# Performance work log

Hardware: AMD Instinct MI355X
Metric: run time of the kernel (lower is better)

## Reference

```python
import jax, jax.numpy as jnp
import numpy as np

N_NODES = 16384
FM = 256
N_EDGES = 524288


def gcn_conv(x, W, b, edge_index, edge_weight):
    """PyG GCNConv: y = D^-1/2 (A+I) D^-1/2 (x @ W) + b, with edge weights."""
    n = x.shape[0]
    loop = jnp.arange(n)
    src = jnp.concatenate([edge_index[0], loop])
    dst = jnp.concatenate([edge_index[1], loop])
    w = jnp.concatenate([edge_weight, jnp.ones((n,), edge_weight.dtype)])
    deg = jax.ops.segment_sum(w, dst, num_segments=n)
    dinv = jnp.where(deg > 0, jax.lax.rsqrt(jnp.maximum(deg, 1e-30)), 0.0)
    norm = dinv[src] * w * dinv[dst]            # [E+n]
    h = x @ W                                    # [n, fm]
    msg = h[src] * norm[:, None]                 # [E+n, fm] gather
    return jax.ops.segment_sum(msg, dst, num_segments=n) + b


def setup_inputs() -> dict:
    key = jax.random.key(0)
    ks = jax.random.split(key, 24)
    inp = {
        "x": jax.random.normal(ks[0], (N_NODES, FM), jnp.float32),
        "edges_f": jax.random.randint(ks[1], (2, N_EDGES), 0, N_NODES),
        "ew_f": jax.random.uniform(ks[2], (N_EDGES,), jnp.float32),
        "edges_s": jax.random.randint(ks[3], (2, N_EDGES), 0, N_NODES),
        "ew_s": jax.random.uniform(ks[4], (N_EDGES,), jnp.float32),
        "edges_g": jax.random.randint(ks[5], (2, N_EDGES), 0, N_NODES),
        "ew_g": jax.random.uniform(ks[6], (N_EDGES,), jnp.float32),
    }
    names = ["f1", "f2", "s1", "s2", "g1", "g2"]
    for i, nm in enumerate(names):
        inp["W" + nm] = 0.05 * jax.random.normal(ks[7 + i], (FM, FM), jnp.float32)
        inp["b" + nm] = jnp.zeros((FM,), jnp.float32)
    inp["fc1_w"] = 0.5 * jax.random.normal(ks[13], (30, 6), jnp.float32)
    inp["fc1_b"] = jnp.zeros((30,), jnp.float32)
    inp["fc2_w"] = 0.5 * jax.random.normal(ks[14], (6, 30), jnp.float32)
    inp["fc2_b"] = jnp.zeros((6,), jnp.float32)
    inp["cnn_w"] = 0.5 * jax.random.normal(ks[15], (6,), jnp.float32)
    inp["cnn_b"] = jnp.zeros((1,), jnp.float32)
    return inp


def reference(x, edges_f, ew_f, edges_s, ew_s, edges_g, ew_g,
              Wf1, bf1, Wf2, bf2, Ws1, bs1, Ws2, bs2, Wg1, bg1, Wg2, bg2,
              fc1_w, fc1_b, fc2_w, fc2_b, cnn_w, cnn_b):
    # three 2-layer GCN branches with relu
    f1 = jax.nn.relu(gcn_conv(x, Wf1, bf1, edges_f, ew_f))
    f2 = jax.nn.relu(gcn_conv(f1, Wf2, bf2, edges_f, ew_f))
    s1 = jax.nn.relu(gcn_conv(x, Ws1, bs1, edges_s, ew_s))
    s2 = jax.nn.relu(gcn_conv(s1, Ws2, bs2, edges_s, ew_s))
    g1 = jax.nn.relu(gcn_conv(x, Wg1, bg1, edges_g, ew_g))
    g2 = jax.nn.relu(gcn_conv(g1, Wg2, bg2, edges_g, ew_g))
    # cat along features then t().view(1,6,fm,N) == stack of transposed branches
    XM = jnp.stack([f1.T, f2.T, s1.T, s2.T, g1.T, g2.T])  # [6, fm, N]
    # SE channel attention
    pooled = jnp.mean(XM, axis=(1, 2))                     # [6]
    h = jax.nn.relu(fc1_w @ pooled + fc1_b)                # [30]
    att = jax.nn.sigmoid(fc2_w @ h + fc2_b)                # [6]
    XM_att = jax.nn.relu(att[:, None, None] * XM)          # [6, fm, N]
    # 1x1 conv 6->1 channels
    out = jnp.einsum('c,cfn->fn', cnn_w, XM_att) + cnn_b[0]  # [fm, N]
    return out.T                                            # [N, fm]
```

## Files before the change

kernel.cpp:

```cpp
#include <hip/hip_runtime.h>
#include <hip/hip_bf16.h>

#define N_NODES 16384
#define FM      256
#define NF      (N_NODES * FM)
#define NF4     (NF / 4)
#define NPART   8
#define NSCAN   (NPART * N_NODES)
#define RS_STRIDE 131076
#define NRS_STRIDE (N_NODES + 2)
#define NCHUNK 128
#define NCHUNK_N 16

typedef __attribute__((ext_vector_type(8))) short short8;
typedef __attribute__((ext_vector_type(8))) ushort ushort8;
typedef __attribute__((ext_vector_type(4))) float f32x4;

__device__ inline ushort f2bf(float f) {
    uint u = __float_as_uint(f);
    return (ushort)((u + 0x7FFFu + ((u >> 16) & 1u)) >> 16);
}
__device__ inline uint pack2bf(float a, float b) {
    return (uint)f2bf(a) | ((uint)f2bf(b) << 16);
}
__device__ inline float bf2f(ushort u) { return __uint_as_float(((uint)u) << 16); }

__global__ void init_kernel(int* __restrict__ cnt3, float* __restrict__ pooled) {
    int i = blockIdx.x * blockDim.x + threadIdx.x;
    int n = 3 * NSCAN;
    if (i < n) cnt3[i] = 0;
    else if (i < n + 6) pooled[i - n] = 0.0f;
}

__global__ void cnt_edges_all(const int* __restrict__ d0, const int* __restrict__ d1,
                              const int* __restrict__ d2,
                              int* __restrict__ cnt3, int E) {
    int t = blockIdx.y;
    const int* dst = (t == 0) ? d0 : (t == 1) ? d1 : d2;
    int part = blockIdx.x & (NPART - 1);
    int* cnt = cnt3 + t * NSCAN + part * N_NODES;
    int e = blockIdx.x * blockDim.x + threadIdx.x;
    if (e < E) atomicAdd(&cnt[dst[e]], 1);
}


__global__ void tot_kernel(const int* __restrict__ cnt3, int* __restrict__ tot3) {
    int i = blockIdx.x * blockDim.x + threadIdx.x;
    if (i >= 3 * N_NODES) return;
    int set = i / N_NODES;
    int node = i - set * N_NODES;
    const int* cnt = cnt3 + set * NSCAN;
    int s = 0;
#pragma unroll
    for (int p = 0; p < NPART; ++p) s += cnt[p * N_NODES + node];
    tot3[i] = s;
}

__global__ __launch_bounds__(1024) void chunk_sum(const int* __restrict__ src,
                                                  long set_stride,
                                                  int* __restrict__ psum,
                                                  int nchunk) {
    int set = blockIdx.y;
    const int* p = src + (size_t)set * set_stride + (size_t)blockIdx.x * 1024;
    __shared__ int lds[1024];
    int t = threadIdx.x;
    lds[t] = p[t];
    __syncthreads();
    for (int off = 512; off > 0; off >>= 1) {
        if (t < off) lds[t] += lds[t + off];
        __syncthreads();
    }
    if (t == 0) psum[set * nchunk + blockIdx.x] = lds[0];
}

__global__ __launch_bounds__(128) void scan_chunks(int* __restrict__ psum,
                                                   int* __restrict__ npsum) {
    __shared__ int lds[128];
    int t = threadIdx.x;
    for (int set = 0; set < 3; ++set) {
        int v = psum[set * NCHUNK + t];
        lds[t] = v;
        __syncthreads();
        for (int off = 1; off < 128; off <<= 1) {
            int u = (t >= off) ? lds[t - off] : 0;
            __syncthreads();
            lds[t] += u;
            __syncthreads();
        }
        psum[set * NCHUNK + t] = lds[t] - v;
        __syncthreads();
    }
    for (int set = 0; set < 3; ++set) {
        int v = (t < NCHUNK_N) ? npsum[set * NCHUNK_N + t] : 0;
        lds[t] = v;
        __syncthreads();
        for (int off = 1; off < NCHUNK_N; off <<= 1) {
            int u = (t >= off && t < NCHUNK_N) ? lds[t - off] : 0;
            __syncthreads();
            if (t < NCHUNK_N) lds[t] += u;
            __syncthreads();
        }
        if (t < NCHUNK_N) npsum[set * NCHUNK_N + t] = lds[t] - v;
        __syncthreads();
    }
}

__global__ __launch_bounds__(1024) void scan_write_rs(const int* __restrict__ cnt3,
                                                      const int* __restrict__ psum,
                                                      int* __restrict__ rowstart3,
                                                      int* __restrict__ cursor3) {
    int set = blockIdx.y;
    int base = psum[set * NCHUNK + blockIdx.x];
    const int* cnt = cnt3 + set * NSCAN + (size_t)blockIdx.x * 1024;
    int* rs = rowstart3 + set * RS_STRIDE + (size_t)blockIdx.x * 1024;
    int* cur = cursor3 + set * NSCAN + (size_t)blockIdx.x * 1024;
    __shared__ int lds[1024];
    int t = threadIdx.x;
    int v = cnt[t];
    lds[t] = v;
    __syncthreads();
    for (int off = 1; off < 1024; off <<= 1) {
        int u = (t >= off) ? lds[t - off] : 0;
        __syncthreads();
        lds[t] += u;
        __syncthreads();
    }
    int pre = base + lds[t] - v;
    rs[t] = pre;
    cur[t] = pre;
    if (blockIdx.x == NCHUNK - 1 && t == 1023)
        rowstart3[set * RS_STRIDE + NSCAN] = base + lds[t];
}

__global__ __launch_bounds__(1024) void scan_write_nrs(const int* __restrict__ tot3,
                                                       const int* __restrict__ npsum,
                                                       int* __restrict__ nodestart3) {
    int set = blockIdx.y;
    int base = npsum[set * NCHUNK_N + blockIdx.x];
    const int* tot = tot3 + (size_t)set * N_NODES + (size_t)blockIdx.x * 1024;
    int* nrs = nodestart3 + set * NRS_STRIDE + (size_t)blockIdx.x * 1024;
    __shared__ int lds[1024];
    int t = threadIdx.x;
    int v = tot[t];
    lds[t] = v;
    __syncthreads();
    for (int off = 1; off < 1024; off <<= 1) {
        int u = (t >= off) ? lds[t - off] : 0;
        __syncthreads();
        lds[t] += u;
        __syncthreads();
    }
    nrs[t] = base + lds[t] - v;
    if (blockIdx.x == NCHUNK_N - 1 && t == 1023)
        nodestart3[set * NRS_STRIDE + N_NODES] = base + lds[t];
}

__global__ void scatter_all(const int* __restrict__ s0, const int* __restrict__ s1,
                            const int* __restrict__ s2,
                            const float* __restrict__ e0, const float* __restrict__ e1,
                            const float* __restrict__ e2,
                            int* __restrict__ cursor3, int2* __restrict__ csr3, int E) {
    int t = blockIdx.y;
    const int* ed = (t == 0) ? s0 : (t == 1) ? s1 : s2;
    const float* ew = (t == 0) ? e0 : (t == 1) ? e1 : e2;
    int part = blockIdx.x & (NPART - 1);
    int* cursor = cursor3 + t * NSCAN + part * N_NODES;
    int2* csr = csr3 + (size_t)t * E;
    int e = blockIdx.x * blockDim.x + threadIdx.x;
    if (e >= E) return;
    int s = ed[e], d = ed[E + e];
    int pos = atomicAdd(&cursor[d], 1);
    csr[pos] = make_int2(s, __float_as_int(ew[e]));
}

__global__ __launch_bounds__(256) void deg_dinv_all(const int2* __restrict__ csr3,
                                                    const int* __restrict__ rowstart3,
                                                    float* __restrict__ dinv3, int E) {
    int t = blockIdx.y;
    const int2* csr = csr3 + (size_t)t * E;
    const int* rs = rowstart3 + t * RS_STRIDE;
    int node = blockIdx.x * 4 + (threadIdx.x >> 6);
    int lane = threadIdx.x & 63;
    int p = lane >> 3;
    int l8 = lane & 7;
    int beg = rs[p * N_NODES + node], end = rs[p * N_NODES + node + 1];
    float s = 0.0f;
    for (int j = beg + l8; j < end; j += 8)
        s += __int_as_float(csr[j].y);
    for (int o = 32; o > 0; o >>= 1) s += __shfl_down(s, o);
    if (lane == 0) dinv3[t * N_NODES + node] = rsqrtf(1.0f + s);
}

__global__ __launch_bounds__(256) void compact_norm_all(const int2* __restrict__ csr3,
                                                        const int* __restrict__ rowstart3,
                                                        const int* __restrict__ nodestart3,
                                                        const float* __restrict__ dinv3,
                                                        int* __restrict__ csrsrc3,
                                                        float* __restrict__ csrnorm3,
                                                        int E) {
    int t = blockIdx.y;
    const int2* src = csr3 + (size_t)t * E;
    const int* prs = rowstart3 + t * RS_STRIDE;
    const int* nrs = nodestart3 + t * NRS_STRIDE;
    const float* dinv = dinv3 + t * N_NODES;
    int* dsrc = csrsrc3 + (size_t)t * E;
    float* dnorm = csrnorm3 + (size_t)t * E;
    int node = blockIdx.x * 4 + (threadIdx.x >> 6);
    int lane = threadIdx.x & 63;
    float din = dinv[node];
    int w = nrs[node];
#pragma unroll
    for (int p = 0; p < NPART; ++p) {
        int beg = prs[p * N_NODES + node];
        int end = prs[p * N_NODES + node + 1];
        for (int j = beg + lane; j < end; j += 64) {
            int2 c = src[j];
            dsrc[w + (j - beg)] = c.x;
            dnorm[w + (j - beg)] = __int_as_float(c.y) * dinv[c.x] * din;
        }
        w += end - beg;
    }
}

__global__ __launch_bounds__(256) void wpack_kernel(const float* __restrict__ w0,
                                                    const float* __restrict__ w1,
                                                    const float* __restrict__ w2,
                                                    const float* __restrict__ w3,
                                                    const float* __restrict__ w4,
                                                    const float* __restrict__ w5,
                                                    ushort* __restrict__ wt) {
    const float* W;
    switch (blockIdx.z) {
        case 0: W = w0; break; case 1: W = w1; break; case 2: W = w2; break;
        case 3: W = w3; break; case 4: W = w4; break; default: W = w5; break;
    }
    __shared__ float tl[16][17];
    int tx = threadIdx.x & 15, ty = threadIdx.x >> 4;
    int k0 = blockIdx.x * 16, n0 = blockIdx.y * 16;
    tl[ty][tx] = W[(size_t)(k0 + ty) * FM + n0 + tx];
    __syncthreads();
    wt[(size_t)blockIdx.z * FM * FM + (size_t)(n0 + ty) * FM + k0 + tx] = f2bf(tl[tx][ty]);
}

__global__ __launch_bounds__(256) void gemm_mfma(const float* __restrict__ A,
                                                 const ushort* __restrict__ WT,
                                                 ushort* __restrict__ C) {
    __shared__ ushort A_lds[128 * 64];

    const int tid = threadIdx.x;
    const int lane = tid & 63;
    const int wid = tid >> 6;
    const int wm = wid >> 1, wn = wid & 1;
    const int bm = blockIdx.x * 128;
    const int bn = blockIdx.y * 64;
    const int l15 = lane & 15;
    const int lg = lane >> 4;

    f32x4 acc[4][2];
#pragma unroll
    for (int i = 0; i < 4; ++i)
#pragma unroll
        for (int n = 0; n < 2; ++n) acc[i][n] = (f32x4){0.f, 0.f, 0.f, 0.f};

    const int srow = tid >> 1;
    const int shk = tid & 1;
    const float* arow_p = &A[(size_t)(bm + srow) * FM + shk * 32];

    for (int k0 = 0; k0 < 256; k0 += 64) {
        {
            const float* ap = arow_p + k0;
#pragma unroll
            for (int g = 0; g < 4; ++g) {
                float4 a0 = *(const float4*)(ap + g * 8);
                float4 a1 = *(const float4*)(ap + g * 8 + 4);
                uint4 pk;
                pk.x = pack2bf(a0.x, a0.y);
                pk.y = pack2bf(a0.z, a0.w);
                pk.z = pack2bf(a1.x, a1.y);
                pk.w = pack2bf(a1.z, a1.w);
                int kk = shk * 32 + g * 8;
                int idx = srow * 64 + (kk ^ ((srow & 7) << 3));
                *(uint4*)&A_lds[idx] = pk;
            }
        }
        __syncthreads();
#pragma unroll
        for (int s = 0; s < 2; ++s) {
            short8 bfrag[2];
#pragma unroll
            for (int n = 0; n < 2; ++n) {
                int col = bn + wn * 32 + n * 16 + l15;
                bfrag[n] = *(const short8*)&WT[(size_t)col * FM + k0 + s * 32 + lg * 8];
            }
#pragma unroll
            for (int i = 0; i < 4; ++i) {
                int row = wm * 64 + i * 16 + l15;
                int kk = s * 32 + lg * 8;
                short8 afrag = *(const short8*)&A_lds[row * 64 + (kk ^ ((row & 7) << 3))];
#pragma unroll
                for (int n = 0; n < 2; ++n)
                    acc[i][n] = __builtin_amdgcn_mfma_f32_16x16x32_bf16(
                        afrag, bfrag[n], acc[i][n], 0, 0, 0);
            }
        }
        __syncthreads();
    }
#pragma unroll
    for (int i = 0; i < 4; ++i) {
#pragma unroll
        for (int n = 0; n < 2; ++n) {
            int col = bn + wn * 32 + n * 16 + l15;
#pragma unroll
            for (int r = 0; r < 4; ++r) {
                int row = bm + wm * 64 + i * 16 + lg * 4 + r;
                C[(size_t)row * FM + col] = f2bf(acc[i][n][r]);
            }
        }
    }
}

__global__ __launch_bounds__(256) void gcn_aggregate_csr(const ushort* __restrict__ h,
                                                         const int* __restrict__ row_start,
                                                         const int* __restrict__ csr_src,
                                                         const float* __restrict__ csr_norm,
                                                         const float* __restrict__ dinv,
                                                         const float* __restrict__ bias,
                                                         float* __restrict__ out) {
    int node = blockIdx.x * 4 + (threadIdx.x >> 6);
    int lane = threadIdx.x & 63;
    const ushort4* hp = (const ushort4*)h;

    float di = dinv[node];
    float sw = di * di;
    ushort4 q = hp[(size_t)node * 64 + lane];
    float4 accA = make_float4(bf2f(q.x) * sw, bf2f(q.y) * sw,
                              bf2f(q.z) * sw, bf2f(q.w) * sw);
    float4 accB = make_float4(0.f, 0.f, 0.f, 0.f);

    int beg = row_start[node];
    int end = row_start[node + 1];
    int j = beg;
    for (; j + 3 < end; j += 4) {
        int s0 = csr_src[j];
        int s1 = csr_src[j + 1];
        int s2 = csr_src[j + 2];
        int s3 = csr_src[j + 3];
        float w0 = csr_norm[j];
        float w1 = csr_norm[j + 1];
        float w2 = csr_norm[j + 2];
        float w3 = csr_norm[j + 3];
        ushort4 q0 = hp[(size_t)s0 * 64 + lane];
        ushort4 q1 = hp[(size_t)s1 * 64 + lane];
        ushort4 q2 = hp[(size_t)s2 * 64 + lane];
        ushort4 q3 = hp[(size_t)s3 * 64 + lane];
        accA.x += w0 * bf2f(q0.x) + w1 * bf2f(q1.x);
        accA.y += w0 * bf2f(q0.y) + w1 * bf2f(q1.y);
        accA.z += w0 * bf2f(q0.z) + w1 * bf2f(q1.z);
        accA.w += w0 * bf2f(q0.w) + w1 * bf2f(q1.w);
        accB.x += w2 * bf2f(q2.x) + w3 * bf2f(q3.x);
        accB.y += w2 * bf2f(q2.y) + w3 * bf2f(q3.y);
        accB.z += w2 * bf2f(q2.z) + w3 * bf2f(q3.z);
        accB.w += w2 * bf2f(q2.w) + w3 * bf2f(q3.w);
    }
    for (; j < end; ++j) {
        int s0 = csr_src[j];
        float w0 = csr_norm[j];
        ushort4 q0 = hp[(size_t)s0 * 64 + lane];
        accA.x += w0 * bf2f(q0.x);
        accA.y += w0 * bf2f(q0.y);
        accA.z += w0 * bf2f(q0.z);
        accA.w += w0 * bf2f(q0.w);
    }
    float4 bb = ((const float4*)bias)[lane];
    float4 acc;
    acc.x = fmaxf(accA.x + accB.x + bb.x, 0.0f);
    acc.y = fmaxf(accA.y + accB.y + bb.y, 0.0f);
    acc.z = fmaxf(accA.z + accB.z + bb.z, 0.0f);
    acc.w = fmaxf(accA.w + accB.w + bb.w, 0.0f);
    ((float4*)out)[(size_t)node * 64 + lane] = acc;
}

__global__ __launch_bounds__(256) void reduce_branch_kernel(const float* __restrict__ br,
                                                            float* __restrict__ pooled) {
    int c = blockIdx.y;
    const float4* p = (const float4*)(br + (size_t)c * NF + (size_t)blockIdx.x * 16384);
    float s = 0.0f;
#pragma unroll
    for (int i = 0; i < 16; ++i) {
        float4 v = p[threadIdx.x + i * 256];
        s += v.x + v.y + v.z + v.w;
    }
    for (int o = 32; o > 0; o >>= 1) s += __shfl_down(s, o);
    __shared__ float wsum[4];
    if ((threadIdx.x & 63) == 0) wsum[threadIdx.x >> 6] = s;
    __syncthreads();
    if (threadIdx.x == 0)
        atomicAdd(&pooled[c], wsum[0] + wsum[1] + wsum[2] + wsum[3]);
}

__global__ void se_kernel(const float* __restrict__ pooled_sum,
                          const float* __restrict__ fc1_w, const float* __restrict__ fc1_b,
                          const float* __restrict__ fc2_w, const float* __restrict__ fc2_b,
                          float* __restrict__ att) {
    __shared__ float p[6];
    __shared__ float hbuf[30];
    int t = threadIdx.x;
    if (t < 6) p[t] = pooled_sum[t] * (1.0f / ((float)N_NODES * (float)FM));
    __syncthreads();
    if (t < 30) {
        float a = fc1_b[t];
#pragma unroll
        for (int c = 0; c < 6; ++c) a += fc1_w[t * 6 + c] * p[c];
        hbuf[t] = fmaxf(a, 0.0f);
    }
    __syncthreads();
    if (t < 6) {
        float a = fc2_b[t];
#pragma unroll
        for (int j = 0; j < 30; ++j) a += fc2_w[t * 30 + j] * hbuf[j];
        att[t] = 1.0f / (1.0f + expf(-a));
    }
}

__global__ void combine_kernel(const float* __restrict__ br,
                               const float* __restrict__ att,
                               const float* __restrict__ cnn_w,
                               const float* __restrict__ cnn_b,
                               float* __restrict__ out, int total4) {
    int i = blockIdx.x * blockDim.x + threadIdx.x;
    if (i >= total4) return;
    float a[6], w[6];
#pragma unroll
    for (int c = 0; c < 6; ++c) { a[c] = att[c]; w[c] = cnn_w[c]; }
    float cb = cnn_b[0];
    float4 acc = make_float4(cb, cb, cb, cb);
#pragma unroll
    for (int c = 0; c < 6; ++c) {
        float4 v = ((const float4*)(br + (size_t)c * NF))[i];
        acc.x += w[c] * fmaxf(a[c] * v.x, 0.0f);
        acc.y += w[c] * fmaxf(a[c] * v.y, 0.0f);
        acc.z += w[c] * fmaxf(a[c] * v.z, 0.0f);
        acc.w += w[c] * fmaxf(a[c] * v.w, 0.0f);
    }
    ((float4*)out)[i] = acc;
}


static void run_conv(const float* in, const ushort* wtp, const float* b,
                     const int* row_start, const int* csr_src, const float* csr_norm,
                     const float* dinv, ushort* h_bf16, float* out,
                     hipStream_t stream) {
    dim3 ggrid(N_NODES / 128, FM / 64);
    gemm_mfma<<<ggrid, 256, 0, stream>>>(in, wtp, h_bf16);
    gcn_aggregate_csr<<<N_NODES / 4, 256, 0, stream>>>(h_bf16, row_start, csr_src,
                                                       csr_norm, dinv, b, out);
}

extern "C" void kernel_launch(void* const* d_in, const int* in_sizes, int n_in,
                              void* d_out, int out_size, void* d_ws, size_t ws_size,
                              hipStream_t stream) {
    const float* x      = (const float*)d_in[0];
    const int*   ed_f   = (const int*)d_in[1];
    const float* ew_f   = (const float*)d_in[2];
    const int*   ed_s   = (const int*)d_in[3];
    const float* ew_s   = (const float*)d_in[4];
    const int*   ed_g   = (const int*)d_in[5];
    const float* ew_g   = (const float*)d_in[6];
    const float* Wf1 = (const float*)d_in[7];  const float* bf1 = (const float*)d_in[8];
    const float* Wf2 = (const float*)d_in[9];  const float* bf2 = (const float*)d_in[10];
    const float* Ws1 = (const float*)d_in[11]; const float* bs1 = (const float*)d_in[12];
    const float* Ws2 = (const float*)d_in[13]; const float* bs2 = (const float*)d_in[14];
    const float* Wg1 = (const float*)d_in[15]; const float* bg1 = (const float*)d_in[16];
    const float* Wg2 = (const float*)d_in[17]; const float* bg2 = (const float*)d_in[18];
    const float* fc1_w = (const float*)d_in[19]; const float* fc1_b = (const float*)d_in[20];
    const float* fc2_w = (const float*)d_in[21]; const float* fc2_b = (const float*)d_in[22];
    const float* cnn_w = (const float*)d_in[23]; const float* cnn_b = (const float*)d_in[24];

    const int E = in_sizes[1] / 2;

    float* ws = (float*)d_ws;
    float* br = ws;
    float* dinv3  = ws + (size_t)6 * NF;
    float* pooled = dinv3 + 3 * N_NODES;
    float* att    = pooled + 8;
    int*   cnt3       = (int*)(att + 8);
    int*   cursor3    = cnt3 + 3 * NSCAN;
    int*   rowstart3  = cursor3 + 3 * NSCAN;
    int*   nodestart3 = rowstart3 + 3 * RS_STRIDE;
    int*   tot3       = nodestart3 + 3 * NRS_STRIDE + 2;
    int*   psum       = tot3 + 3 * N_NODES;
    int*   npsum      = psum + 3 * NCHUNK;
    int2*  csr3       = (int2*)(npsum + 3 * NCHUNK_N + 8);
    int*   csr_src3   = (int*)(csr3 + (size_t)3 * E);
    float* csr_norm3  = (float*)(csr_src3 + (size_t)3 * E);
    ushort* wt        = (ushort*)(csr_norm3 + (size_t)3 * E);

    float* dinv_set[3] = { dinv3, dinv3 + N_NODES, dinv3 + 2 * N_NODES };
    int*   nrs_set[3]  = { nodestart3, nodestart3 + NRS_STRIDE,
                           nodestart3 + 2 * NRS_STRIDE };
    int*   csrc_set[3] = { csr_src3, csr_src3 + E, csr_src3 + 2 * E };
    float* cnorm_set[3] = { csr_norm3, csr_norm3 + E, csr_norm3 + 2 * E };

    float* f1 = br + (size_t)0 * NF;
    float* f2 = br + (size_t)1 * NF;
    float* s1 = br + (size_t)2 * NF;
    float* s2 = br + (size_t)3 * NF;
    float* g1 = br + (size_t)4 * NF;
    float* g2 = br + (size_t)5 * NF;

    ushort* h = (ushort*)d_out;

    init_kernel<<<(3 * NSCAN + 6 + 255) / 256, 256, 0, stream>>>(cnt3, pooled);
    {
        dim3 g((E + 255) / 256, 3);
        cnt_edges_all<<<g, 256, 0, stream>>>(ed_f + E, ed_s + E, ed_g + E, cnt3, E);
    }
    tot_kernel<<<(3 * N_NODES + 255) / 256, 256, 0, stream>>>(cnt3, tot3);
    {
        dim3 g1d(NCHUNK, 3);
        chunk_sum<<<g1d, 1024, 0, stream>>>(cnt3, (long)NSCAN, psum, NCHUNK);
        dim3 g2d(NCHUNK_N, 3);
        chunk_sum<<<g2d, 1024, 0, stream>>>(tot3, (long)N_NODES, npsum, NCHUNK_N);
    }
    scan_chunks<<<1, 128, 0, stream>>>(psum, npsum);
    {
        dim3 g1d(NCHUNK, 3);
        scan_write_rs<<<g1d, 1024, 0, stream>>>(cnt3, psum, rowstart3, cursor3);
        dim3 g2d(NCHUNK_N, 3);
        scan_write_nrs<<<g2d, 1024, 0, stream>>>(tot3, npsum, nodestart3);
    }
    {
        dim3 g((E + 255) / 256, 3);
        scatter_all<<<g, 256, 0, stream>>>(ed_f, ed_s, ed_g, ew_f, ew_s, ew_g,
                                           cursor3, csr3, E);
    }
    {
        dim3 g(N_NODES / 4, 3);
        deg_dinv_all<<<g, 256, 0, stream>>>(csr3, rowstart3, dinv3, E);
    }
    {
        dim3 g(N_NODES / 4, 3);
        compact_norm_all<<<g, 256, 0, stream>>>(csr3, rowstart3, nodestart3, dinv3,
                                                csr_src3, csr_norm3, E);
    }
    {
        dim3 wg(16, 16, 6);
        wpack_kernel<<<wg, 256, 0, stream>>>(Wf1, Wf2, Ws1, Ws2, Wg1, Wg2, wt);
    }
    const ushort* wt_set[6] = { wt, wt + 65536, wt + 2 * 65536,
                                wt + 3 * 65536, wt + 4 * 65536, wt + 5 * 65536 };

    run_conv(x,  wt_set[0], bf1, nrs_set[0], csrc_set[0], cnorm_set[0], dinv_set[0], h, f1, stream);
    run_conv(f1, wt_set[1], bf2, nrs_set[0], csrc_set[0], cnorm_set[0], dinv_set[0], h, f2, stream);
    run_conv(x,  wt_set[2], bs1, nrs_set[1], csrc_set[1], cnorm_set[1], dinv_set[1], h, s1, stream);
    run_conv(s1, wt_set[3], bs2, nrs_set[1], csrc_set[1], cnorm_set[1], dinv_set[1], h, s2, stream);
    run_conv(x,  wt_set[4], bg1, nrs_set[2], csrc_set[2], cnorm_set[2], dinv_set[2], h, g1, stream);
    run_conv(g1, wt_set[5], bg2, nrs_set[2], csrc_set[2], cnorm_set[2], dinv_set[2], h, g2, stream);

    dim3 rgrid(256, 6);
    reduce_branch_kernel<<<rgrid, 256, 0, stream>>>(br, pooled);
    se_kernel<<<1, 64, 0, stream>>>(pooled, fc1_w, fc1_b, fc2_w, fc2_b, att);

    combine_kernel<<<NF4 / 256, 256, 0, stream>>>(br, att, cnn_w, cnn_b,
                                                  (float*)d_out, NF4);
}
```

Baseline: 578.8 us.

## Store branch activations in bf16, fuse pooling into aggregation, pre-convert x

```diff
diff --git a/kernel.cpp b/kernel.cpp
--- a/kernel.cpp
+++ b/kernel.cpp
@@ -40,7 +40,7 @@
     int part = blockIdx.x & (NPART - 1);
     int* cnt = cnt3 + t * NSCAN + part * N_NODES;
     int e = blockIdx.x * blockDim.x + threadIdx.x;
-    if (e < E) atomicAdd(&cnt[dst[e]], 1);
+    if (e < E) atomicAdd(&cnt[__builtin_nontemporal_load(&dst[e])], 1);
 }
 
 
@@ -168,9 +168,11 @@
     int2* csr = csr3 + (size_t)t * E;
     int e = blockIdx.x * blockDim.x + threadIdx.x;
     if (e >= E) return;
-    int s = ed[e], d = ed[E + e];
+    int s = __builtin_nontemporal_load(&ed[e]);
+    int d = __builtin_nontemporal_load(&ed[E + e]);
+    float w = __builtin_nontemporal_load(&ew[e]);
     int pos = atomicAdd(&cursor[d], 1);
-    csr[pos] = make_int2(s, __float_as_int(ew[e]));
+    csr[pos] = make_int2(s, __float_as_int(w));
 }
 
 __global__ __launch_bounds__(256) void deg_dinv_all(const int2* __restrict__ csr3,
@@ -242,7 +244,20 @@
     wt[(size_t)blockIdx.z * FM * FM + (size_t)(n0 + ty) * FM + k0 + tx] = f2bf(tl[tx][ty]);
 }
 
-__global__ __launch_bounds__(256) void gemm_mfma(const float* __restrict__ A,
+__global__ void x2bf_kernel(const float* __restrict__ x, ushort* __restrict__ xb) {
+    int i = blockIdx.x * blockDim.x + threadIdx.x;
+    if (i >= NF / 8) return;
+    const float4* xp = (const float4*)x;
+    float4 a = xp[2 * i], b = xp[2 * i + 1];
+    uint4 pk;
+    pk.x = pack2bf(a.x, a.y);
+    pk.y = pack2bf(a.z, a.w);
+    pk.z = pack2bf(b.x, b.y);
+    pk.w = pack2bf(b.z, b.w);
+    ((uint4*)xb)[i] = pk;
+}
+
+__global__ __launch_bounds__(256) void gemm_mfma(const ushort* __restrict__ A,
                                                  const ushort* __restrict__ WT,
                                                  ushort* __restrict__ C) {
     __shared__ ushort A_lds[128 * 64];
@@ -264,23 +279,17 @@
 
     const int srow = tid >> 1;
     const int shk = tid & 1;
-    const float* arow_p = &A[(size_t)(bm + srow) * FM + shk * 32];
+    const ushort* arow_p = &A[(size_t)(bm + srow) * FM + shk * 32];
 
     for (int k0 = 0; k0 < 256; k0 += 64) {
         {
-            const float* ap = arow_p + k0;
+            const ushort* ap = arow_p + k0;
 #pragma unroll
             for (int g = 0; g < 4; ++g) {
-                float4 a0 = *(const float4*)(ap + g * 8);
-                float4 a1 = *(const float4*)(ap + g * 8 + 4);
-                uint4 pk;
-                pk.x = pack2bf(a0.x, a0.y);
-                pk.y = pack2bf(a0.z, a0.w);
-                pk.z = pack2bf(a1.x, a1.y);
-                pk.w = pack2bf(a1.z, a1.w);
+                ushort8 v = *(const ushort8*)(ap + g * 8);
                 int kk = shk * 32 + g * 8;
                 int idx = srow * 64 + (kk ^ ((srow & 7) << 3));
-                *(uint4*)&A_lds[idx] = pk;
+                *(ushort8*)&A_lds[idx] = v;
             }
         }
         __syncthreads();
@@ -325,7 +334,9 @@
                                                          const float* __restrict__ csr_norm,
                                                          const float* __restrict__ dinv,
                                                          const float* __restrict__ bias,
-                                                         float* __restrict__ out) {
+                                                         ushort* __restrict__ out,
+                                                         float* __restrict__ pooled,
+                                                         int bidx) {
     int node = blockIdx.x * 4 + (threadIdx.x >> 6);
     int lane = threadIdx.x & 63;
     const ushort4* hp = (const ushort4*)h;
@@ -372,30 +383,22 @@
         accA.w += w0 * bf2f(q0.w);
     }
     float4 bb = ((const float4*)bias)[lane];
-    float4 acc;
-    acc.x = fmaxf(accA.x + accB.x + bb.x, 0.0f);
-    acc.y = fmaxf(accA.y + accB.y + bb.y, 0.0f);
-    acc.z = fmaxf(accA.z + accB.z + bb.z, 0.0f);
-    acc.w = fmaxf(accA.w + accB.w + bb.w, 0.0f);
-    ((float4*)out)[(size_t)node * 64 + lane] = acc;
-}
-
-__global__ __launch_bounds__(256) void reduce_branch_kernel(const float* __restrict__ br,
-                                                            float* __restrict__ pooled) {
-    int c = blockIdx.y;
-    const float4* p = (const float4*)(br + (size_t)c * NF + (size_t)blockIdx.x * 16384);
-    float s = 0.0f;
-#pragma unroll
-    for (int i = 0; i < 16; ++i) {
-        float4 v = p[threadIdx.x + i * 256];
-        s += v.x + v.y + v.z + v.w;
-    }
-    for (int o = 32; o > 0; o >>= 1) s += __shfl_down(s, o);
+    float4 r;
+    r.x = fmaxf(accA.x + accB.x + bb.x, 0.0f);
+    r.y = fmaxf(accA.y + accB.y + bb.y, 0.0f);
+    r.z = fmaxf(accA.z + accB.z + bb.z, 0.0f);
+    r.w = fmaxf(accA.w + accB.w + bb.w, 0.0f);
+    ushort4 o;
+    o.x = f2bf(r.x); o.y = f2bf(r.y); o.z = f2bf(r.z); o.w = f2bf(r.w);
+    ((ushort4*)out)[(size_t)node * 64 + lane] = o;
+
+    float psum = r.x + r.y + r.z + r.w;
+    for (int o2 = 32; o2 > 0; o2 >>= 1) psum += __shfl_down(psum, o2);
     __shared__ float wsum[4];
-    if ((threadIdx.x & 63) == 0) wsum[threadIdx.x >> 6] = s;
+    if (lane == 0) wsum[threadIdx.x >> 6] = psum;
     __syncthreads();
     if (threadIdx.x == 0)
-        atomicAdd(&pooled[c], wsum[0] + wsum[1] + wsum[2] + wsum[3]);
+        atomicAdd(&pooled[bidx], wsum[0] + wsum[1] + wsum[2] + wsum[3]);
 }
 
 __global__ void se_kernel(const float* __restrict__ pooled_sum,
@@ -422,7 +425,7 @@
     }
 }
 
-__global__ void combine_kernel(const float* __restrict__ br,
+__global__ void combine_kernel(const ushort* __restrict__ br,
                                const float* __restrict__ att,
                                const float* __restrict__ cnn_w,
                                const float* __restrict__ cnn_b,
@@ -436,24 +439,25 @@
     float4 acc = make_float4(cb, cb, cb, cb);
 #pragma unroll
     for (int c = 0; c < 6; ++c) {
-        float4 v = ((const float4*)(br + (size_t)c * NF))[i];
-        acc.x += w[c] * fmaxf(a[c] * v.x, 0.0f);
-        acc.y += w[c] * fmaxf(a[c] * v.y, 0.0f);
-        acc.z += w[c] * fmaxf(a[c] * v.z, 0.0f);
-        acc.w += w[c] * fmaxf(a[c] * v.w, 0.0f);
+        ushort4 q = ((const ushort4*)(br + (size_t)c * NF))[i];
+        acc.x += w[c] * fmaxf(a[c] * bf2f(q.x), 0.0f);
+        acc.y += w[c] * fmaxf(a[c] * bf2f(q.y), 0.0f);
+        acc.z += w[c] * fmaxf(a[c] * bf2f(q.z), 0.0f);
+        acc.w += w[c] * fmaxf(a[c] * bf2f(q.w), 0.0f);
     }
     ((float4*)out)[i] = acc;
 }
 
 
-static void run_conv(const float* in, const ushort* wtp, const float* b,
+static void run_conv(const ushort* inA, const ushort* wtp, const float* b,
                      const int* row_start, const int* csr_src, const float* csr_norm,
-                     const float* dinv, ushort* h_bf16, float* out,
-                     hipStream_t stream) {
+                     const float* dinv, ushort* h_bf16, ushort* out,
+                     float* pooled, int bidx, hipStream_t stream) {
     dim3 ggrid(N_NODES / 128, FM / 64);
-    gemm_mfma<<<ggrid, 256, 0, stream>>>(in, wtp, h_bf16);
+    gemm_mfma<<<ggrid, 256, 0, stream>>>(inA, wtp, h_bf16);
     gcn_aggregate_csr<<<N_NODES / 4, 256, 0, stream>>>(h_bf16, row_start, csr_src,
-                                                       csr_norm, dinv, b, out);
+                                                       csr_norm, dinv, b, out,
+                                                       pooled, bidx);
 }
 
 extern "C" void kernel_launch(void* const* d_in, const int* in_sizes, int n_in,
@@ -478,22 +482,22 @@
 
     const int E = in_sizes[1] / 2;
 
-    float* ws = (float*)d_ws;
-    float* br = ws;
-    float* dinv3  = ws + (size_t)6 * NF;
-    float* pooled = dinv3 + 3 * N_NODES;
-    float* att    = pooled + 8;
-    int*   cnt3       = (int*)(att + 8);
-    int*   cursor3    = cnt3 + 3 * NSCAN;
-    int*   rowstart3  = cursor3 + 3 * NSCAN;
-    int*   nodestart3 = rowstart3 + 3 * RS_STRIDE;
-    int*   tot3       = nodestart3 + 3 * NRS_STRIDE + 2;
-    int*   psum       = tot3 + 3 * N_NODES;
-    int*   npsum      = psum + 3 * NCHUNK;
-    int2*  csr3       = (int2*)(npsum + 3 * NCHUNK_N + 8);
-    int*   csr_src3   = (int*)(csr3 + (size_t)3 * E);
-    float* csr_norm3  = (float*)(csr_src3 + (size_t)3 * E);
-    ushort* wt        = (ushort*)(csr_norm3 + (size_t)3 * E);
+    ushort* br_u = (ushort*)d_ws;
+    ushort* xb   = br_u + (size_t)6 * NF;
+    ushort* wt   = xb + NF;
+    float*  dinv3  = (float*)(wt + 6 * FM * FM);
+    float*  pooled = dinv3 + 3 * N_NODES;
+    float*  att    = pooled + 8;
+    int*    cnt3       = (int*)(att + 8);
+    int*    cursor3    = cnt3 + 3 * NSCAN;
+    int*    rowstart3  = cursor3 + 3 * NSCAN;
+    int*    nodestart3 = rowstart3 + 3 * RS_STRIDE;
+    int*    tot3       = nodestart3 + 3 * NRS_STRIDE + 2;
+    int*    psum       = tot3 + 3 * N_NODES;
+    int*    npsum      = psum + 3 * NCHUNK;
+    int2*   csr3       = (int2*)(npsum + 3 * NCHUNK_N + 8);
+    int*    csr_src3   = (int*)(csr3 + (size_t)3 * E);
+    float*  csr_norm3  = (float*)(csr_src3 + (size_t)3 * E);
 
     float* dinv_set[3] = { dinv3, dinv3 + N_NODES, dinv3 + 2 * N_NODES };
     int*   nrs_set[3]  = { nodestart3, nodestart3 + NRS_STRIDE,
@@ -501,12 +505,12 @@
     int*   csrc_set[3] = { csr_src3, csr_src3 + E, csr_src3 + 2 * E };
     float* cnorm_set[3] = { csr_norm3, csr_norm3 + E, csr_norm3 + 2 * E };
 
-    float* f1 = br + (size_t)0 * NF;
-    float* f2 = br + (size_t)1 * NF;
-    float* s1 = br + (size_t)2 * NF;
-    float* s2 = br + (size_t)3 * NF;
-    float* g1 = br + (size_t)4 * NF;
-    float* g2 = br + (size_t)5 * NF;
+    ushort* f1 = br_u + (size_t)0 * NF;
+    ushort* f2 = br_u + (size_t)1 * NF;
+    ushort* s1 = br_u + (size_t)2 * NF;
+    ushort* s2 = br_u + (size_t)3 * NF;
+    ushort* g1 = br_u + (size_t)4 * NF;
+    ushort* g2 = br_u + (size_t)5 * NF;
 
     ushort* h = (ushort*)d_out;
 
@@ -547,20 +551,20 @@
         dim3 wg(16, 16, 6);
         wpack_kernel<<<wg, 256, 0, stream>>>(Wf1, Wf2, Ws1, Ws2, Wg1, Wg2, wt);
     }
+    x2bf_kernel<<<(NF / 8 + 255) / 256, 256, 0, stream>>>(x, xb);
+
     const ushort* wt_set[6] = { wt, wt + 65536, wt + 2 * 65536,
                                 wt + 3 * 65536, wt + 4 * 65536, wt + 5 * 65536 };
 
-    run_conv(x,  wt_set[0], bf1, nrs_set[0], csrc_set[0], cnorm_set[0], dinv_set[0], h, f1, stream);
-    run_conv(f1, wt_set[1], bf2, nrs_set[0], csrc_set[0], cnorm_set[0], dinv_set[0], h, f2, stream);
-    run_conv(x,  wt_set[2], bs1, nrs_set[1], csrc_set[1], cnorm_set[1], dinv_set[1], h, s1, stream);
-    run_conv(s1, wt_set[3], bs2, nrs_set[1], csrc_set[1], cnorm_set[1], dinv_set[1], h, s2, stream);
-    run_conv(x,  wt_set[4], bg1, nrs_set[2], csrc_set[2], cnorm_set[2], dinv_set[2], h, g1, stream);
-    run_conv(g1, wt_set[5], bg2, nrs_set[2], csrc_set[2], cnorm_set[2], dinv_set[2], h, g2, stream);
-
-    dim3 rgrid(256, 6);
-    reduce_branch_kernel<<<rgrid, 256, 0, stream>>>(br, pooled);
+    run_conv(xb, wt_set[0], bf1, nrs_set[0], csrc_set[0], cnorm_set[0], dinv_set[0], h, f1, pooled, 0, stream);
+    run_conv(f1, wt_set[1], bf2, nrs_set[0], csrc_set[0], cnorm_set[0], dinv_set[0], h, f2, pooled, 1, stream);
+    run_conv(xb, wt_set[2], bs1, nrs_set[1], csrc_set[1], cnorm_set[1], dinv_set[1], h, s1, pooled, 2, stream);
+    run_conv(s1, wt_set[3], bs2, nrs_set[1], csrc_set[1], cnorm_set[1], dinv_set[1], h, s2, pooled, 3, stream);
+    run_conv(xb, wt_set[4], bg1, nrs_set[2], csrc_set[2], cnorm_set[2], dinv_set[2], h, g1, pooled, 4, stream);
+    run_conv(g1, wt_set[5], bg2, nrs_set[2], csrc_set[2], cnorm_set[2], dinv_set[2], h, g2, pooled, 5, stream);
+
     se_kernel<<<1, 64, 0, stream>>>(pooled, fc1_w, fc1_b, fc2_w, fc2_b, att);
 
-    combine_kernel<<<NF4 / 256, 256, 0, stream>>>(br, att, cnn_w, cnn_b,
+    combine_kernel<<<NF4 / 256, 256, 0, stream>>>(br_u, att, cnn_w, cnn_b,
                                                   (float*)d_out, NF4);
 }
```

Result: slower. 729.4 us (+26.0%).
